# Performance work log

Hardware: AMD Instinct MI355X
Metric: run time of the kernel (lower is better)

## Reference

```python
import jax, jax.numpy as jnp
import numpy as np

EPS = 1e-5


def layer_norm(x, g, b):
    mu = jnp.mean(x, axis=-1, keepdims=True)
    var = jnp.var(x, axis=-1, keepdims=True)
    return (x - mu) * jax.lax.rsqrt(var + EPS) * g + b


def setup_inputs() -> dict:
    key = jax.random.key(0)
    ks = jax.random.split(key, 10)
    B, N, D, H, DFF = 4, 2048, 384, 6, 2048
    s = lambda fan: 1.0 / np.sqrt(fan)
    return {
        "x": jax.random.normal(ks[0], (B, N, D), dtype=jnp.float32),
        "norm_g": jnp.ones((D,), jnp.float32),
        "norm_b": jnp.zeros((D,), jnp.float32),
        "w_qkv": jax.random.uniform(ks[1], (D, 3 * D), jnp.float32, -s(D), s(D)),
        "b_qkv": jax.random.uniform(ks[2], (3 * D,), jnp.float32, -s(D), s(D)),
        "w1": jax.random.uniform(ks[3], (D, DFF), jnp.float32, -s(D), s(D)),
        "b1": jax.random.uniform(ks[4], (DFF,), jnp.float32, -s(D), s(D)),
        "w2": jax.random.uniform(ks[5], (DFF, D), jnp.float32, -s(DFF), s(DFF)),
        "b2": jax.random.uniform(ks[6], (D,), jnp.float32, -s(DFF), s(DFF)),
    }


def reference(x, norm_g, norm_b, w_qkv, b_qkv, w1, b1, w2, b2):
    H = 6
    B, N, D = x.shape
    hd = D // H
    scale = hd ** -0.5

    # --- attention (pre-norm, shared LayerNorm params) ---
    out = layer_norm(x, norm_g, norm_b)
    qkv = out @ w_qkv + b_qkv                     # [B, N, 3D]
    q, k, v = jnp.split(qkv, 3, axis=-1)
    to_heads = lambda t: t.reshape(B, N, H, hd).transpose(0, 2, 1, 3)  # b h n d
    q, k, v = to_heads(q), to_heads(k), to_heads(v)
    scores = jnp.einsum('bhid,bhjd->bhij', q, k) * scale
    attn = jax.nn.softmax(scores, axis=-1)        # dropout is identity in eval
    att = jnp.einsum('bhij,bhjd->bhid', attn, v)  # [B, H, N, hd]
    att = att.transpose(0, 2, 1, 3).reshape(B, N, D)
    x2 = x + att

    # --- MLP (same shared LayerNorm) ---
    y = layer_norm(x2, norm_g, norm_b)
    h = jax.nn.gelu(y @ w1 + b1, approximate=False)  # torch F.gelu exact
    mlp = h @ w2 + b2
    return x2 + mlp
```

## Files before the change

kernel.cpp:

```cpp
#include <hip/hip_runtime.h>
#include <cstdint>
#include <cstddef>

#define DEV static __device__ __forceinline__

typedef __attribute__((ext_vector_type(8))) short short8;
typedef __attribute__((ext_vector_type(4))) float f32x4;
typedef __attribute__((ext_vector_type(4))) unsigned short u16x4;
typedef __attribute__((ext_vector_type(2))) unsigned short u16x2;

constexpr int kB = 4, kN = 2048, kD = 384, kH = 6, kDFF = 2048;
constexpr int kM = kB * kN;
constexpr float kQPre = 0.18033688011112042f;

DEV float exp2fast(float f) { return __builtin_amdgcn_exp2f(f); }

DEV unsigned short f2b(float f) {
  union { float fp; uint32_t u; } v; v.fp = f;
  return (unsigned short)((v.u + 0x7fffu + ((v.u >> 16) & 1u)) >> 16);
}

DEV void gload16(const unsigned short* g, unsigned short* l) {
  __builtin_amdgcn_global_load_lds(
      (const __attribute__((address_space(1))) unsigned int*)g,
      (__attribute__((address_space(3))) unsigned int*)l, 16, 0, 0);
}

__global__ __launch_bounds__(256) void k_transpose(
    const float* __restrict__ w, unsigned short* __restrict__ wT, int K, int Nn) {
  __shared__ unsigned short t[64][66];
  const int nbk = K >> 6;
  const int bk = blockIdx.x % nbk, bn = blockIdx.x / nbk;
  const int k0 = bk << 6, n0 = bn << 6;
  const int tid = threadIdx.x;
  const int cl = tid & 63, rw = tid >> 6;
#pragma unroll
  for (int it = 0; it < 16; ++it) {
    int kk = it * 4 + rw;
    t[cl][kk] = f2b(w[(size_t)(k0 + kk) * Nn + n0 + cl]);
  }
  __syncthreads();
  const int kq = (tid & 15) << 2;
  const int nr = tid >> 4;
#pragma unroll
  for (int it = 0; it < 4; ++it) {
    int nn = it * 16 + nr;
    u16x4 v;
    v[0] = t[nn][kq]; v[1] = t[nn][kq + 1]; v[2] = t[nn][kq + 2]; v[3] = t[nn][kq + 3];
    *(u16x4*)&wT[(size_t)(n0 + nn) * K + k0 + kq] = v;
  }
}

__global__ __launch_bounds__(256) void k_layernorm(
    const float* __restrict__ x, const float* __restrict__ g,
    const float* __restrict__ bta, unsigned short* __restrict__ y) {
  int row  = blockIdx.x * 4 + (threadIdx.x >> 6);
  int lane = threadIdx.x & 63;
  const float* xr = x + (size_t)row * kD;
  float4 a = *(const float4*)(xr + lane * 4);
  float2 c = *(const float2*)(xr + 256 + lane * 2);
  float s  = a.x + a.y + a.z + a.w + c.x + c.y;
  float ss = a.x*a.x + a.y*a.y + a.z*a.z + a.w*a.w + c.x*c.x + c.y*c.y;
#pragma unroll
  for (int m = 1; m < 64; m <<= 1) {
    s  += __shfl_xor(s,  m, 64);
    ss += __shfl_xor(ss, m, 64);
  }
  float mean = s * (1.0f / kD);
  float var  = ss * (1.0f / kD) - mean * mean;
  float r = rsqrtf(var + 1e-5f);
  float4 g4 = *(const float4*)(g + lane * 4);
  float2 g2 = *(const float2*)(g + 256 + lane * 2);
  float4 b4 = *(const float4*)(bta + lane * 4);
  float2 b2 = *(const float2*)(bta + 256 + lane * 2);
  unsigned short* yr = y + (size_t)row * kD;
  u16x4 o4;
  o4[0] = f2b((a.x - mean) * r * g4.x + b4.x);
  o4[1] = f2b((a.y - mean) * r * g4.y + b4.y);
  o4[2] = f2b((a.z - mean) * r * g4.z + b4.z);
  o4[3] = f2b((a.w - mean) * r * g4.w + b4.w);
  *(u16x4*)(yr + lane * 4) = o4;
  u16x2 o2;
  o2[0] = f2b((c.x - mean) * r * g2.x + b2.x);
  o2[1] = f2b((c.y - mean) * r * g2.y + b2.y);
  *(u16x2*)(yr + 256 + lane * 2) = o2;
}

template <int MODE, int TM>
__global__ __launch_bounds__(256) void k_gemm(
    const unsigned short* __restrict__ A, const unsigned short* __restrict__ Bt,
    const float* __restrict__ bias, int K, int Nn, int nbm,
    unsigned short* __restrict__ oq, unsigned short* __restrict__ okk,
    unsigned short* __restrict__ ov, unsigned short* __restrict__ oh,
    const float* __restrict__ res, float* __restrict__ out) {
  constexpr int MI = TM / 32;
  __shared__ unsigned short lA[2][TM * 32];
  __shared__ unsigned short lB[2][128 * 32];
  const int tid = threadIdx.x, wid = tid >> 6, lane = tid & 63;
  const int bm = blockIdx.x % nbm, bn = blockIdx.x / nbm;
  const int m0 = bm * TM, n0 = bn * 128;
  const int wr = wid >> 1, wc = wid & 1;
  const int wmo = wr * (TM >> 1);
  const int lr16 = lane & 15, lq = lane >> 4;
  const int gsw = ((lr16 >> 1) & 3) << 3;

  f32x4 acc[MI][4];
#pragma unroll
  for (int i = 0; i < MI; i++)
#pragma unroll
    for (int j = 0; j < 4; j++) acc[i][j] = f32x4{0.f, 0.f, 0.f, 0.f};

  const int srow = (lane >> 2);
  const int scc  = (lane & 3) << 3;

  auto stage = [&](int buf, int k0) {
#pragma unroll
    for (int p = 0; p < TM / 64; p++) {
      int row = ((wid + (p << 2)) << 4) + srow;
      int sl  = ((lane & 3) ^ ((row >> 1) & 3)) << 3;
      gload16(A + (size_t)(m0 + row) * K + k0 + sl, &lA[buf][(row << 5) + scc]);
    }
#pragma unroll
    for (int p = 0; p < 2; p++) {
      int row = ((wid + (p << 2)) << 4) + srow;
      int sl  = ((lane & 3) ^ ((row >> 1) & 3)) << 3;
      gload16(Bt + (size_t)(n0 + row) * K + k0 + sl, &lB[buf][(row << 5) + scc]);
    }
  };

  stage(0, 0);

  const int nkt = K >> 5;
  for (int kt = 0; kt < nkt; ++kt) {
    const int cur = kt & 1;
    __syncthreads();
    if (kt + 1 < nkt) stage(cur ^ 1, (kt + 1) << 5);
    short8 af[MI], bf[4];
#pragma unroll
    for (int i = 0; i < MI; i++)
      af[i] = *(const short8*)&lA[cur][(wmo + (i << 4) + lr16) * 32 + ((lq << 3) ^ gsw)];
#pragma unroll
    for (int j = 0; j < 4; j++)
      bf[j] = *(const short8*)&lB[cur][((wc << 6) + (j << 4) + lr16) * 32 + ((lq << 3) ^ gsw)];
#pragma unroll
    for (int i = 0; i < MI; i++)
#pragma unroll
      for (int j = 0; j < 4; j++)
        acc[i][j] = __builtin_amdgcn_mfma_f32_16x16x32_bf16(af[i], bf[j], acc[i][j], 0, 0, 0);
  }

#pragma unroll
  for (int i = 0; i < MI; i++) {
    int mbase = m0 + wmo + (i << 4) + (lq << 2);
#pragma unroll
    for (int j = 0; j < 4; j++) {
      int col = n0 + (wc << 6) + (j << 4) + lr16;
      float bv = bias[col];
#pragma unroll
      for (int rr = 0; rr < 4; ++rr) {
        float cvl = acc[i][j][rr] + bv;
        int m = mbase + rr;
        if (MODE == 0) {
          int bI = m >> 11, nI = m & 2047;
          if (col < 384) {
            int hh = col >> 6, dd = col & 63;
            oq[(((size_t)bI * kH + hh) * kN + nI) * 64 + dd] = f2b(cvl * kQPre);
          } else if (col < 768) {
            int c2 = col - 384; int hh = c2 >> 6, dd = c2 & 63;
            okk[(((size_t)bI * kH + hh) * kN + nI) * 64 + dd] = f2b(cvl);
          } else {
            int c2 = col - 768; int hh = c2 >> 6, dd = c2 & 63;
            ov[(((size_t)bI * kH + hh) * 64 + dd) * kN + nI] = f2b(cvl);
          }
        } else if (MODE == 1) {
          float gl = 0.5f * cvl * (1.0f + erff(cvl * 0.70710678118654752f));
          oh[(size_t)m * kDFF + col] = f2b(gl);
        } else {
          size_t idx = (size_t)m * kD + col;
          out[idx] = res[idx] + cvl;
        }
      }
    }
  }
}

__global__ __launch_bounds__(256) void k_attn(
    const unsigned short* __restrict__ Q, const unsigned short* __restrict__ Kg,
    const unsigned short* __restrict__ Vt, const float* __restrict__ x,
    float* __restrict__ x2) {
  __shared__ unsigned short lK[2][64 * 64];
  __shared__ unsigned short lV[2][64 * 64];
  __shared__ unsigned short lP[4][16 * 64];
  const int tid = threadIdx.x, wid = tid >> 6, lane = tid & 63;
  const int bh = blockIdx.x >> 5, qt = blockIdx.x & 31;
  const int b = bh / kH, h = bh - b * kH;
  const unsigned short* Qp = Q  + (size_t)bh * kN * 64;
  const unsigned short* Kp = Kg + (size_t)bh * kN * 64;
  const unsigned short* Vp = Vt + (size_t)bh * 64 * kN;
  const int lr16 = lane & 15, lq = lane >> 4;
  const int q0w = qt * 64 + wid * 16;
  const int rsw = (lr16 & 7) << 3;

  const int sr  = ((wid << 3) + (lane >> 3));
  const int scc = (lane & 7) << 3;

  short8 qf[2];
#pragma unroll
  for (int ks = 0; ks < 2; ++ks)
    qf[ks] = *(const short8*)(Qp + (size_t)(q0w + lr16) * 64 + ks * 32 + lq * 8);

  float l_r = 0.f;
  f32x4 o[4];
#pragma unroll
  for (int df = 0; df < 4; ++df) o[df] = f32x4{0.f, 0.f, 0.f, 0.f};

  auto stage = [&](int buf, int t) {
#pragma unroll
    for (int p = 0; p < 2; p++) {
      int r = sr + (p << 5);
      int sl = ((lane & 7) ^ (r & 7)) << 3;
      gload16(Kp + (size_t)(t * 64 + r) * 64 + sl, &lK[buf][(r << 6) + scc]);
      gload16(Vp + (size_t)r * kN + t * 64 + sl,   &lV[buf][(r << 6) + scc]);
    }
  };

  stage(0, 0);

  constexpr int kNT = kN / 64;
  for (int t = 0; t < kNT; ++t) {
    const int cur = t & 1;
    __syncthreads();
    if (t + 1 < kNT) stage(cur ^ 1, t + 1);

    f32x4 s4[4];
#pragma unroll
    for (int j = 0; j < 4; j++) {
      s4[j] = f32x4{0.f, 0.f, 0.f, 0.f};
#pragma unroll
      for (int ks = 0; ks < 2; ks++) {
        short8 kf = *(const short8*)&lK[cur][((j << 4) + lr16) * 64 + ((ks * 32 + (lq << 3)) ^ rsw)];
        s4[j] = __builtin_amdgcn_mfma_f32_16x16x32_bf16(kf, qf[ks], s4[j], 0, 0, 0);
      }
    }

    float pj[4][4], js[4];
#pragma unroll
    for (int j = 0; j < 4; j++) {
#pragma unroll
      for (int rr = 0; rr < 4; rr++) pj[j][rr] = exp2fast(s4[j][rr] - 4.0f);
      js[j] = (pj[j][0] + pj[j][1]) + (pj[j][2] + pj[j][3]);
    }
    float psum = (js[0] + js[1]) + (js[2] + js[3]);
    psum += __shfl_xor(psum, 16, 64);
    psum += __shfl_xor(psum, 32, 64);
    l_r += psum;

#pragma unroll
    for (int j = 0; j < 4; j++) {
      uint32_t w0, w1;
      asm("v_cvt_pk_bf16_f32 %0, %1, %2" : "=v"(w0) : "v"(pj[j][0]), "v"(pj[j][1]));
      asm("v_cvt_pk_bf16_f32 %0, %1, %2" : "=v"(w1) : "v"(pj[j][2]), "v"(pj[j][3]));
      int kvb = (j << 4) + (lq << 2);
      uint2 wv; wv.x = w0; wv.y = w1;
      *(uint2*)&lP[wid][(lr16 << 6) + (kvb ^ rsw)] = wv;
    }
    short8 pa[2];
#pragma unroll
    for (int ks = 0; ks < 2; ks++)
      pa[ks] = *(const short8*)&lP[wid][(lr16 << 6) + ((ks * 32 + (lq << 3)) ^ rsw)];
#pragma unroll
    for (int df = 0; df < 4; df++) {
#pragma unroll
      for (int ks = 0; ks < 2; ks++) {
        short8 vf = *(const short8*)&lV[cur][((df << 4) + lr16) * 64 + ((ks * 32 + (lq << 3)) ^ rsw)];
        o[df] = __builtin_amdgcn_mfma_f32_16x16x32_bf16(pa[ks], vf, o[df], 0, 0, 0);
      }
    }
  }

  float inv = 1.0f / l_r;
  float invr[4];
#pragma unroll
  for (int rr = 0; rr < 4; rr++) invr[rr] = __shfl(inv, (lq << 2) + rr, 16);
#pragma unroll
  for (int df = 0; df < 4; df++)
#pragma unroll
    for (int rr = 0; rr < 4; rr++) {
      int row  = q0w + (lq << 2) + rr;
      int colD = h * 64 + (df << 4) + lr16;
      size_t idx = ((size_t)(b * kN + row)) * kD + colD;
      x2[idx] = x[idx] + o[df][rr] * invr[rr];
    }
}

extern "C" void kernel_launch(void* const* d_in, const int* in_sizes, int n_in,
                              void* d_out, int out_size, void* d_ws, size_t ws_size,
                              hipStream_t stream) {
  const float* x    = (const float*)d_in[0];
  const float* ng   = (const float*)d_in[1];
  const float* nb   = (const float*)d_in[2];
  const float* wqkv = (const float*)d_in[3];
  const float* bqkv = (const float*)d_in[4];
  const float* w1   = (const float*)d_in[5];
  const float* b1   = (const float*)d_in[6];
  const float* w2   = (const float*)d_in[7];
  const float* b2   = (const float*)d_in[8];
  float* out = (float*)d_out;

  char* p = (char*)d_ws;
  auto take = [&](size_t bytes) -> char* {
    char* r = p; p += (bytes + 255) & ~(size_t)255; return r;
  };
  unsigned short* y     = (unsigned short*)take((size_t)kM * kD * 2);
  unsigned short* wqkvT = (unsigned short*)take((size_t)3 * kD * kD * 2);
  unsigned short* w1T   = (unsigned short*)take((size_t)kDFF * kD * 2);
  unsigned short* w2T   = (unsigned short*)take((size_t)kD * kDFF * 2);
  unsigned short* Qw    = (unsigned short*)take((size_t)kM * kD * 2);
  unsigned short* Kw    = (unsigned short*)take((size_t)kM * kD * 2);
  unsigned short* Vtw   = (unsigned short*)take((size_t)kM * kD * 2);
  float*          x2    = (float*)take((size_t)kM * kD * 4);
  unsigned short* hbuf  = (unsigned short*)take((size_t)kM * kDFF * 2);

  k_transpose<<<(kD / 64) * (3 * kD / 64), 256, 0, stream>>>(wqkv, wqkvT, kD, 3 * kD);
  k_transpose<<<(kD / 64) * (kDFF / 64), 256, 0, stream>>>(w1, w1T, kD, kDFF);
  k_transpose<<<(kDFF / 64) * (kD / 64), 256, 0, stream>>>(w2, w2T, kDFF, kD);

  k_layernorm<<<kM / 4, 256, 0, stream>>>(x, ng, nb, y);
  k_gemm<0, 128><<<64 * 9, 256, 0, stream>>>(y, wqkvT, bqkv, kD, 3 * kD, 64,
                                             Qw, Kw, Vtw, nullptr, nullptr, nullptr);
  k_attn<<<kB * kH * (kN / 64), 256, 0, stream>>>(Qw, Kw, Vtw, x, x2);
  k_layernorm<<<kM / 4, 256, 0, stream>>>(x2, ng, nb, y);
  k_gemm<1, 128><<<64 * 16, 256, 0, stream>>>(y, w1T, b1, kD, kDFF, 64,
                                              nullptr, nullptr, nullptr, hbuf, nullptr, nullptr);
  k_gemm<2, 64><<<128 * 3, 256, 0, stream>>>(hbuf, w2T, b2, kDFF, kD, 128,
                                             nullptr, nullptr, nullptr, nullptr, x2, out);
}
```

Before: 164.2 us.

## Split attention KV range in two halves and combine partials in a new kernel

The attention kernel now splits each (batch, head, query-tile) job into two blocks, each covering half of the key/value sequence. Each block writes unnormalized fp32 partial outputs and row sums into scratch space reused from the MLP hidden buffer. A new combine kernel adds the two partials, normalizes them and adds the residual to form x2. This doubles the grid to improve CU occupancy and load balance, at the cost of an extra launch and roughly 25 MB of extra fp32 partial traffic written and read back.

```diff
diff --git a/kernel.cpp b/kernel.cpp
--- a/kernel.cpp
+++ b/kernel.cpp
@@ -11,6 +11,7 @@
 
 constexpr int kB = 4, kN = 2048, kD = 384, kH = 6, kDFF = 2048;
 constexpr int kM = kB * kN;
+constexpr int kBH = kB * kH;
 constexpr float kQPre = 0.18033688011112042f;
 
 DEV float exp2fast(float f) { return __builtin_amdgcn_exp2f(f); }
@@ -186,17 +187,20 @@
 
 __global__ __launch_bounds__(256) void k_attn(
     const unsigned short* __restrict__ Q, const unsigned short* __restrict__ Kg,
-    const unsigned short* __restrict__ Vt, const float* __restrict__ x,
-    float* __restrict__ x2) {
+    const unsigned short* __restrict__ Vt,
+    float* __restrict__ Opart, float* __restrict__ lpart) {
   __shared__ unsigned short lK[2][64 * 64];
   __shared__ unsigned short lV[2][64 * 64];
   __shared__ unsigned short lP[4][16 * 64];
   const int tid = threadIdx.x, wid = tid >> 6, lane = tid & 63;
-  const int bh = blockIdx.x >> 5, qt = blockIdx.x & 31;
-  const int b = bh / kH, h = bh - b * kH;
+  int rem = blockIdx.x;
+  const int half = rem >= (kBH * 32) ? 1 : 0;
+  rem -= half * (kBH * 32);
+  const int bh = rem >> 5, qt = rem & 31;
+  const int kv0 = half << 10;
   const unsigned short* Qp = Q  + (size_t)bh * kN * 64;
-  const unsigned short* Kp = Kg + (size_t)bh * kN * 64;
-  const unsigned short* Vp = Vt + (size_t)bh * 64 * kN;
+  const unsigned short* Kp = Kg + ((size_t)bh * kN + kv0) * 64;
+  const unsigned short* Vp = Vt + (size_t)bh * 64 * kN + kv0;
   const int lr16 = lane & 15, lq = lane >> 4;
   const int q0w = qt * 64 + wid * 16;
   const int rsw = (lr16 & 7) << 3;
@@ -226,7 +230,7 @@
 
   stage(0, 0);
 
-  constexpr int kNT = kN / 64;
+  constexpr int kNT = (kN / 2) / 64;
   for (int t = 0; t < kNT; ++t) {
     const int cur = t & 1;
     __syncthreads();
@@ -278,19 +282,35 @@
     }
   }
 
-  float inv = 1.0f / l_r;
-  float invr[4];
-#pragma unroll
-  for (int rr = 0; rr < 4; rr++) invr[rr] = __shfl(inv, (lq << 2) + rr, 16);
+  const size_t obase = ((size_t)(half * kBH + bh) * kN + q0w);
 #pragma unroll
   for (int df = 0; df < 4; df++)
 #pragma unroll
     for (int rr = 0; rr < 4; rr++) {
-      int row  = q0w + (lq << 2) + rr;
-      int colD = h * 64 + (df << 4) + lr16;
-      size_t idx = ((size_t)(b * kN + row)) * kD + colD;
-      x2[idx] = x[idx] + o[df][rr] * invr[rr];
-    }
+      int qrow = (lq << 2) + rr;
+      Opart[(obase + qrow) * 64 + (df << 4) + lr16] = o[df][rr];
+    }
+  if (lane < 16) lpart[(size_t)(half * kBH + bh) * kN + q0w + lane] = l_r;
+}
+
+__global__ __launch_bounds__(256) void k_combine(
+    const float* __restrict__ Opart, const float* __restrict__ lpart,
+    const float* __restrict__ x, float* __restrict__ x2) {
+  const int row  = blockIdx.x * 4 + (threadIdx.x >> 6);
+  const int lane = threadIdx.x & 63;
+  const int b = row >> 11, n = row & 2047;
+  const float* xr = x + (size_t)row * kD;
+  float* x2r = x2 + (size_t)row * kD;
+#pragma unroll
+  for (int h = 0; h < kH; ++h) {
+    const int bh = b * kH + h;
+    size_t i0 = ((size_t)bh * kN + n) * 64 + lane;
+    size_t i1 = ((size_t)(bh + kBH) * kN + n) * 64 + lane;
+    float l0 = lpart[(size_t)bh * kN + n];
+    float l1 = lpart[(size_t)(bh + kBH) * kN + n];
+    float v = (Opart[i0] + Opart[i1]) * (1.0f / (l0 + l1));
+    x2r[h * 64 + lane] = xr[h * 64 + lane] + v;
+  }
 }
 
 extern "C" void kernel_launch(void* const* d_in, const int* in_sizes, int n_in,
@@ -320,6 +340,8 @@
   unsigned short* Vtw   = (unsigned short*)take((size_t)kM * kD * 2);
   float*          x2    = (float*)take((size_t)kM * kD * 4);
   unsigned short* hbuf  = (unsigned short*)take((size_t)kM * kDFF * 2);
+  float* Opart = (float*)hbuf;
+  float* lpart = Opart + (size_t)2 * kBH * kN * 64;
 
   k_transpose<<<(kD / 64) * (3 * kD / 64), 256, 0, stream>>>(wqkv, wqkvT, kD, 3 * kD);
   k_transpose<<<(kD / 64) * (kDFF / 64), 256, 0, stream>>>(w1, w1T, kD, kDFF);
@@ -328,7 +350,8 @@
   k_layernorm<<<kM / 4, 256, 0, stream>>>(x, ng, nb, y);
   k_gemm<0, 128><<<64 * 9, 256, 0, stream>>>(y, wqkvT, bqkv, kD, 3 * kD, 64,
                                              Qw, Kw, Vtw, nullptr, nullptr, nullptr);
-  k_attn<<<kB * kH * (kN / 64), 256, 0, stream>>>(Qw, Kw, Vtw, x, x2);
+  k_attn<<<2 * kBH * 32, 256, 0, stream>>>(Qw, Kw, Vtw, Opart, lpart);
+  k_combine<<<kM / 4, 256, 0, stream>>>(Opart, lpart, x, x2);
   k_layernorm<<<kM / 4, 256, 0, stream>>>(x2, ng, nb, y);
   k_gemm<1, 128><<<64 * 16, 256, 0, stream>>>(y, w1T, b1, kD, kDFF, 64,
                                               nullptr, nullptr, nullptr, hbuf, nullptr, nullptr);
```

New measurement: 170.1 us. 3.6% more time.
